# Kernel optimization log

Hardware: AMD Instinct MI355X
Metric: run time of the kernel (lower is better)

Reference implementation:

```python
import jax, jax.numpy as jnp
import numpy as np

B = 65536            # batch of configurations
F = 32               # num_frames (joints)
DOF = 29             # controllable joints
# tree: chain 0..29, two mimic branches off frame 10; parent index always < child -> topo order = range(F)
PARENTS = [-1] + list(range(29)) + [10, 10]


def _np_rodrigues(w):
    th = np.linalg.norm(w)
    if th < 1e-12:
        return np.eye(3)
    k = w / th
    K = np.array([[0, -k[2], k[1]], [k[2], 0, -k[0]], [-k[1], k[0], 0]])
    return np.eye(3) + np.sin(th) * K + (1 - np.cos(th)) * (K @ K)


def setup_inputs() -> dict:
    key = jax.random.key(0)
    rng = np.random.default_rng(0)
    # joint types: 0 fixed, 1 revolute, 2 prismatic
    types = np.ones(F, dtype=np.int32)
    types[0] = 0
    types[15] = 2
    types[22] = 2
    # controllable = non-fixed, non-mimic (mimic dst = 30, 31)
    ctrl = np.array([i for i in range(F) if types[i] != 0 and i not in (30, 31)], dtype=np.int32)
    assert ctrl.shape[0] == DOF
    axes = rng.normal(size=(F, 3)).astype(np.float32)
    axes /= np.linalg.norm(axes, axis=-1, keepdims=True)
    origins = np.tile(np.eye(4, dtype=np.float32), (F, 1, 1))
    for i in range(F):
        origins[i, :3, :3] = _np_rodrigues(rng.normal(size=3) * 0.5)
        origins[i, :3, 3] = rng.normal(size=3) * 0.1
    joint_angles = jax.random.normal(key, (B, DOF), dtype=jnp.float32)
    return {
        "joint_angles": joint_angles,
        "all_axes": jnp.asarray(axes),
        "all_origins": jnp.asarray(origins),
        "mimic_multipliers": jnp.array([1.0, -1.0], dtype=jnp.float32),
        "mimic_offsets": jnp.array([0.1, -0.1], dtype=jnp.float32),
        "ctrlable_indices": jnp.asarray(ctrl),
        "mimic_src_indices": jnp.array([5, 6], dtype=jnp.int32),
        "mimic_dst_indices": jnp.array([30, 31], dtype=jnp.int32),
        "joint_types": jnp.asarray(types),
    }


def exp_map(w):
    # axis-angle (...,3) -> rotation (...,3,3), Rodrigues, eps-safe at w=0
    theta = jnp.sqrt(jnp.sum(w * w, axis=-1, keepdims=True) + 1e-18)  # (...,1)
    k = w / theta
    kx, ky, kz = k[..., 0], k[..., 1], k[..., 2]
    zero = jnp.zeros_like(kx)
    K = jnp.stack(
        [jnp.stack([zero, -kz, ky], -1),
         jnp.stack([kz, zero, -kx], -1),
         jnp.stack([-ky, kx, zero], -1)], -2)
    st = jnp.sin(theta)[..., None]
    ct = jnp.cos(theta)[..., None]
    return jnp.eye(3, dtype=w.dtype) + st * K + (1.0 - ct) * (K @ K)


def _fk(joint_angles, all_axes, all_origins, mimic_multipliers, mimic_offsets,
        ctrlable_indices, mimic_src_indices, mimic_dst_indices, joint_types):
    b = joint_angles.shape[0]
    # scatter controllable angles, then mimic gather/scatter
    all_angles = jnp.zeros((b, F), joint_angles.dtype).at[:, ctrlable_indices].set(joint_angles)
    mimic_vals = all_angles[:, mimic_src_indices] * mimic_multipliers + mimic_offsets
    all_angles = all_angles.at[:, mimic_dst_indices].set(mimic_vals)
    # per-frame local motion (B,F,4,4)
    w = all_axes[None, :, :] * all_angles[..., None]          # (B,F,3)
    R = exp_map(w)                                            # (B,F,3,3)
    R = jnp.where((joint_types == 1)[None, :, None, None], R, jnp.eye(3, dtype=w.dtype))
    t = jnp.where((joint_types == 2)[None, :, None], w, jnp.zeros((), w.dtype))
    top = jnp.concatenate([R, t[..., None]], axis=-1)         # (B,F,3,4)
    bottom = jnp.broadcast_to(jnp.array([0, 0, 0, 1], w.dtype), (b, F, 1, 4))
    motion = jnp.concatenate([top, bottom], axis=-2)          # (B,F,4,4)
    local = jnp.einsum('fij,bfjk->bfik', all_origins, motion)
    # sequential tree-structured compose (F is small & static -> unrolled)
    poses = []
    for i in range(F):
        p = PARENTS[i]
        li = local[:, i]
        poses.append(li if p < 0 else poses[p] @ li)
    return jnp.stack(poses, axis=1)                            # (B,F,4,4)


def reference(joint_angles, all_axes, all_origins, mimic_multipliers, mimic_offsets,
              ctrlable_indices, mimic_src_indices, mimic_dst_indices, joint_types):
    return _fk(joint_angles, all_axes, all_origins, mimic_multipliers, mimic_offsets,
               ctrlable_indices, mimic_src_indices, mimic_dst_indices, joint_types)
```

## Files before the change

### kernel.cpp

```cpp
#include <hip/hip_runtime.h>
#include <math.h>

#define NF 32
#define NDOF 29
#define BLOCK 256
#define SLOT_DW 20

__device__ __forceinline__ void amul(float* __restrict__ N,
                                     const float* __restrict__ A,
                                     const float* __restrict__ B) {
    #pragma unroll
    for (int r = 0; r < 3; ++r) {
        const float a0 = A[r*4+0], a1 = A[r*4+1], a2 = A[r*4+2], a3 = A[r*4+3];
        N[r*4+0] = a0*B[0] + a1*B[4] + a2*B[8];
        N[r*4+1] = a0*B[1] + a1*B[5] + a2*B[9];
        N[r*4+2] = a0*B[2] + a1*B[6] + a2*B[10];
        N[r*4+3] = a0*B[3] + a1*B[7] + a2*B[11] + a3;
    }
}

__global__ __launch_bounds__(BLOCK) void fk_kernel(
    const float* __restrict__ ja,
    const float* __restrict__ axes,
    const float* __restrict__ origins,
    const float* __restrict__ mmul,
    const float* __restrict__ moff,
    const int*   __restrict__ ctrl,
    const int*   __restrict__ msrc,
    const int*   __restrict__ mdst,
    const int*   __restrict__ types,
    float*       __restrict__ out,
    int B)
{
    __shared__ float s_ax[NF][3];
    __shared__ float s_or[NF][12];
    __shared__ int   s_type[NF];
    __shared__ int   s_slot[NF];
    __shared__ float s_mult[NF];
    __shared__ float s_off[NF];
    __shared__ float s_stage[4][64 * SLOT_DW];

    const int tid  = threadIdx.x;
    const int lane = tid & 63;
    const int wv   = tid >> 6;
    const int sub  = lane & 7;
    const int grp  = lane & ~7;

    if (tid < NF) {
        const int f = tid;
        s_ax[f][0] = axes[f*3+0];
        s_ax[f][1] = axes[f*3+1];
        s_ax[f][2] = axes[f*3+2];
        #pragma unroll
        for (int i = 0; i < 12; ++i) s_or[f][i] = origins[f*16 + i];
        s_type[f] = types[f];
        int slot = -1;
        for (int j = 0; j < NDOF; ++j) if (ctrl[j] == f) slot = j;
        float mu = 1.0f, of = 0.0f;
        for (int m = 0; m < 2; ++m) {
            if (mdst[m] == f) {
                const int sf = msrc[m];
                for (int j = 0; j < NDOF; ++j) if (ctrl[j] == sf) slot = j;
                mu = mmul[m]; of = moff[m];
            }
        }
        s_slot[f] = slot; s_mult[f] = mu; s_off[f] = of;
    }
    __syncthreads();

    const long bat = (long)blockIdx.x * 32 + (tid >> 3);
    const bool bok = bat < (long)B;

    float M[4][12];
    #pragma unroll
    for (int j = 0; j < 4; ++j) {
        const int f    = 4*sub + j;
        const int slot = s_slot[f];
        float a = 0.0f;
        if (slot >= 0 && bok) a = fmaf(s_mult[f], ja[bat * NDOF + slot], s_off[f]);
        const float wx = a * s_ax[f][0];
        const float wy = a * s_ax[f][1];
        const float wz = a * s_ax[f][2];
        const int ty = s_type[f];
        float R0,R1,R2,R3,R4,R5,R6,R7,R8;
        if (ty == 1) {
            const float t2 = wx*wx + wy*wy + wz*wz;
            const float th = sqrtf(t2 + 1e-18f);
            const float inv = 1.0f / th;
            const float kx = wx*inv, ky = wy*inv, kz = wz*inv;
            float s, c;
            __sincosf(th, &s, &c);
            const float v = 1.0f - c;
            R0 = fmaf(v*kx, kx, c);
            R1 = v*kx*ky - s*kz;
            R2 = v*kx*kz + s*ky;
            R3 = v*kx*ky + s*kz;
            R4 = fmaf(v*ky, ky, c);
            R5 = v*ky*kz - s*kx;
            R6 = v*kx*kz - s*ky;
            R7 = v*ky*kz + s*kx;
            R8 = fmaf(v*kz, kz, c);
        } else {
            R0=1.f;R1=0.f;R2=0.f;R3=0.f;R4=1.f;R5=0.f;R6=0.f;R7=0.f;R8=1.f;
        }
        const float tx  = (ty == 2) ? wx : 0.0f;
        const float tyv = (ty == 2) ? wy : 0.0f;
        const float tz  = (ty == 2) ? wz : 0.0f;
        const float* O = s_or[f];
        #pragma unroll
        for (int r = 0; r < 3; ++r) {
            const float o0 = O[r*4+0], o1 = O[r*4+1], o2 = O[r*4+2], o3 = O[r*4+3];
            M[j][r*4+0] = o0*R0 + o1*R3 + o2*R6;
            M[j][r*4+1] = o0*R1 + o1*R4 + o2*R7;
            M[j][r*4+2] = o0*R2 + o1*R5 + o2*R8;
            M[j][r*4+3] = o0*tx + o1*tyv + o2*tz + o3;
        }
    }

    float I[12];
    #pragma unroll
    for (int i = 0; i < 12; ++i) I[i] = M[0][i];
    #pragma unroll
    for (int j = 1; j < 4; ++j) {
        float N[12];
        amul(N, I, M[j]);
        const bool keep = !(sub == 7 && j >= 2);
        #pragma unroll
        for (int i = 0; i < 12; ++i) I[i] = keep ? N[i] : I[i];
    }

    #pragma unroll
    for (int d = 1; d <= 4; d <<= 1) {
        const int src = grp | ((sub - d) & 7);
        float T[12];
        #pragma unroll
        for (int i = 0; i < 12; ++i) T[i] = __shfl(I[i], src, 64);
        float N[12];
        amul(N, T, I);
        const bool use = (sub >= d);
        #pragma unroll
        for (int i = 0; i < 12; ++i) I[i] = use ? N[i] : I[i];
    }

    const float ID[12] = {1,0,0,0, 0,1,0,0, 0,0,1,0};
    float run[12];
    {
        const int src = grp | ((sub - 1) & 7);
        #pragma unroll
        for (int i = 0; i < 12; ++i) {
            const float t = __shfl(I[i], src, 64);
            run[i] = (sub > 0) ? t : ID[i];
        }
    }

    float P10[12];
    #pragma unroll
    for (int i = 0; i < 12; ++i) P10[i] = run[i];
    #pragma unroll
    for (int j = 0; j < 4; ++j) {
        float N[12];
        amul(N, run, M[j]);
        const bool chain = !(sub == 7 && j >= 2);
        #pragma unroll
        for (int i = 0; i < 12; ++i) {
            M[j][i] = chain ? N[i] : M[j][i];
            run[i]  = chain ? N[i] : run[i];
        }
        if (j == 2 && sub == 2) {
            #pragma unroll
            for (int i = 0; i < 12; ++i) P10[i] = N[i];
        }
    }
    #pragma unroll
    for (int i = 0; i < 12; ++i) P10[i] = __shfl(P10[i], grp | 2, 64);
    #pragma unroll
    for (int j = 2; j < 4; ++j) {
        float N[12];
        amul(N, P10, M[j]);
        #pragma unroll
        for (int i = 0; i < 12; ++i) M[j][i] = (sub == 7) ? N[i] : M[j][i];
    }

    float* const st = s_stage[wv];
    const long wbat0 = (long)blockIdx.x * 32 + wv * 8;
    float4* const out4 = (float4*)out;
    const int row = lane & 3;

    #pragma unroll
    for (int j = 0; j < 4; ++j) {
        float4* wp = (float4*)&st[lane * SLOT_DW];
        wp[0] = make_float4(M[j][0], M[j][1], M[j][2],  M[j][3]);
        wp[1] = make_float4(M[j][4], M[j][5], M[j][6],  M[j][7]);
        wp[2] = make_float4(M[j][8], M[j][9], M[j][10], M[j][11]);
        wp[3] = make_float4(0.0f, 0.0f, 0.0f, 1.0f);
        __builtin_amdgcn_wave_barrier();
        #pragma unroll
        for (int m = 0; m < 4; ++m) {
            const int  slot = m * 16 + (lane >> 2);
            const float4 v  = *(const float4*)&st[slot * SLOT_DW + row * 4];
            const long bb   = wbat0 + (slot >> 3);
            const int  fr   = 4 * (slot & 7) + j;
            if (bb < (long)B)
                out4[bb * 128 + fr * 4 + row] = v;
        }
        __builtin_amdgcn_wave_barrier();
    }
}

extern "C" void kernel_launch(void* const* d_in, const int* in_sizes, int n_in,
                              void* d_out, int out_size, void* d_ws, size_t ws_size,
                              hipStream_t stream) {
    const float* ja   = (const float*)d_in[0];
    const float* axes = (const float*)d_in[1];
    const float* orig = (const float*)d_in[2];
    const float* mmul = (const float*)d_in[3];
    const float* moff = (const float*)d_in[4];
    const int*   ctrl = (const int*)d_in[5];
    const int*   msrc = (const int*)d_in[6];
    const int*   mdst = (const int*)d_in[7];
    const int*   typs = (const int*)d_in[8];
    float* out = (float*)d_out;

    const int B = in_sizes[0] / NDOF;
    const int grid = (B + 31) / 32;
    fk_kernel<<<grid, BLOCK, 0, stream>>>(ja, axes, orig, mmul, moff,
                                          ctrl, msrc, mdst, typs, out, B);
}
```

Baseline: 164.0 us.

## Recompute local transforms instead of holding four matrices in registers

Keeps only the four joint angles live and rebuilds each local 3x4 transform (Rodrigues plus origin multiply) when it is needed, once for the prefix scan and again in the final chaining and store pass. The mimic-branch fix-up is folded into the store loop. This frees the 48-float M array so register pressure drops and occupancy may rise. The cost is doubled sincos and matrix-build arithmetic per joint.

```diff
diff --git a/kernel.cpp b/kernel.cpp
--- a/kernel.cpp
+++ b/kernel.cpp
@@ -71,13 +71,18 @@
     const long bat = (long)blockIdx.x * 32 + (tid >> 3);
     const bool bok = bat < (long)B;
 
-    float M[4][12];
+    float ang[4];
     #pragma unroll
     for (int j = 0; j < 4; ++j) {
         const int f    = 4*sub + j;
         const int slot = s_slot[f];
-        float a = 0.0f;
-        if (slot >= 0 && bok) a = fmaf(s_mult[f], ja[bat * NDOF + slot], s_off[f]);
+        ang[j] = (slot >= 0 && bok)
+               ? fmaf(s_mult[f], ja[bat * NDOF + slot], s_off[f]) : 0.0f;
+    }
+
+    auto build = [&](int j, float* __restrict__ L) {
+        const int f = 4*sub + j;
+        const float a  = ang[j];
         const float wx = a * s_ax[f][0];
         const float wy = a * s_ax[f][1];
         const float wz = a * s_ax[f][2];
@@ -110,23 +115,28 @@
         #pragma unroll
         for (int r = 0; r < 3; ++r) {
             const float o0 = O[r*4+0], o1 = O[r*4+1], o2 = O[r*4+2], o3 = O[r*4+3];
-            M[j][r*4+0] = o0*R0 + o1*R3 + o2*R6;
-            M[j][r*4+1] = o0*R1 + o1*R4 + o2*R7;
-            M[j][r*4+2] = o0*R2 + o1*R5 + o2*R8;
-            M[j][r*4+3] = o0*tx + o1*tyv + o2*tz + o3;
-        }
-    }
+            L[r*4+0] = o0*R0 + o1*R3 + o2*R6;
+            L[r*4+1] = o0*R1 + o1*R4 + o2*R7;
+            L[r*4+2] = o0*R2 + o1*R5 + o2*R8;
+            L[r*4+3] = o0*tx + o1*tyv + o2*tz + o3;
+        }
+    };
 
     float I[12];
-    #pragma unroll
-    for (int i = 0; i < 12; ++i) I[i] = M[0][i];
-    #pragma unroll
-    for (int j = 1; j < 4; ++j) {
-        float N[12];
-        amul(N, I, M[j]);
-        const bool keep = !(sub == 7 && j >= 2);
-        #pragma unroll
-        for (int i = 0; i < 12; ++i) I[i] = keep ? N[i] : I[i];
+    {
+        float L[12];
+        build(0, L);
+        #pragma unroll
+        for (int i = 0; i < 12; ++i) I[i] = L[i];
+        #pragma unroll
+        for (int j = 1; j < 4; ++j) {
+            build(j, L);
+            float N[12];
+            amul(N, I, L);
+            const bool keep = !(sub == 7 && j >= 2);
+            #pragma unroll
+            for (int i = 0; i < 12; ++i) I[i] = keep ? N[i] : I[i];
+        }
     }
 
     #pragma unroll
@@ -153,45 +163,46 @@
         }
     }
 
-    float P10[12];
-    #pragma unroll
-    for (int i = 0; i < 12; ++i) P10[i] = run[i];
-    #pragma unroll
-    for (int j = 0; j < 4; ++j) {
-        float N[12];
-        amul(N, run, M[j]);
-        const bool chain = !(sub == 7 && j >= 2);
-        #pragma unroll
-        for (int i = 0; i < 12; ++i) {
-            M[j][i] = chain ? N[i] : M[j][i];
-            run[i]  = chain ? N[i] : run[i];
-        }
-        if (j == 2 && sub == 2) {
-            #pragma unroll
-            for (int i = 0; i < 12; ++i) P10[i] = N[i];
-        }
-    }
-    #pragma unroll
-    for (int i = 0; i < 12; ++i) P10[i] = __shfl(P10[i], grp | 2, 64);
-    #pragma unroll
-    for (int j = 2; j < 4; ++j) {
-        float N[12];
-        amul(N, P10, M[j]);
-        #pragma unroll
-        for (int i = 0; i < 12; ++i) M[j][i] = (sub == 7) ? N[i] : M[j][i];
-    }
-
     float* const st = s_stage[wv];
     const long wbat0 = (long)blockIdx.x * 32 + wv * 8;
     float4* const out4 = (float4*)out;
     const int row = lane & 3;
 
+    float P10[12];
+    #pragma unroll
+    for (int i = 0; i < 12; ++i) P10[i] = 0.0f;
+
     #pragma unroll
     for (int j = 0; j < 4; ++j) {
+        float L[12];
+        build(j, L);
+        float N[12];
+        amul(N, run, L);
+
+        if (j == 2) {
+            #pragma unroll
+            for (int i = 0; i < 12; ++i) P10[i] = __shfl(N[i], grp | 2, 64);
+        }
+
+        float pose[12];
+        if (j < 2) {
+            #pragma unroll
+            for (int i = 0; i < 12; ++i) pose[i] = N[i];
+        } else {
+            float Lf[12];
+            amul(Lf, P10, L);
+            #pragma unroll
+            for (int i = 0; i < 12; ++i) pose[i] = (sub == 7) ? Lf[i] : N[i];
+        }
+
+        const bool chain = !(sub == 7 && j >= 2);
+        #pragma unroll
+        for (int i = 0; i < 12; ++i) run[i] = chain ? N[i] : run[i];
+
         float4* wp = (float4*)&st[lane * SLOT_DW];
-        wp[0] = make_float4(M[j][0], M[j][1], M[j][2],  M[j][3]);
-        wp[1] = make_float4(M[j][4], M[j][5], M[j][6],  M[j][7]);
-        wp[2] = make_float4(M[j][8], M[j][9], M[j][10], M[j][11]);
+        wp[0] = make_float4(pose[0], pose[1], pose[2],  pose[3]);
+        wp[1] = make_float4(pose[4], pose[5], pose[6],  pose[7]);
+        wp[2] = make_float4(pose[8], pose[9], pose[10], pose[11]);
         wp[3] = make_float4(0.0f, 0.0f, 0.0f, 1.0f);
         __builtin_amdgcn_wave_barrier();
         #pragma unroll
```

Result: slower. 168.1 us (+2.5%).
